# Kernel optimization log

Hardware: AMD Instinct MI355X
Metric: run time of the kernel (lower is better)

The kernel has to match this reference:

```python
import jax, jax.numpy as jnp
import numpy as np

KERNEL = 3
STRIDE = 1

def _unfold(x, k, s):
    # torch.nn.Unfold: output [B, C*k*k, P] with (c, kh, kw) flattened channel-major
    B, C, H, W = x.shape
    oh = (H - k) // s + 1
    ow = (W - k) // s + 1
    cols = []
    for di in range(k):
        for dj in range(k):
            cols.append(x[:, :, di:di + oh * s:s, dj:dj + ow * s:s])
    p = jnp.stack(cols, axis=2)            # [B, C, k*k, oh, ow]
    return p.reshape(B, C * k * k, oh * ow), oh, ow

def setup_inputs() -> dict:
    key = jax.random.key(0)
    k1, k2 = jax.random.split(key)
    B, C, H, W = 32, 96, 32, 32
    out_c, k, s = 96, KERNEL, STRIDE
    oh = (H - k) // s + 1
    ow = (W - k) // s + 1
    P = oh * ow
    x = jax.random.normal(k1, (B, C, H, W), dtype=jnp.float32)
    weight = jax.random.normal(k2, (P, out_c, C * k * k), dtype=jnp.float32) * 0.01
    bias = jnp.zeros((P, out_c), dtype=jnp.float32)
    return {"x": x, "weight": weight, "bias": bias}

def reference(x, weight, bias):
    B = x.shape[0]
    out_c = weight.shape[1]
    patches, oh, ow = _unfold(x, KERNEL, STRIDE)          # [B, K, P]
    # per-patch distinct weights: out[b,p,o] = sum_k patches[b,k,p] * weight[p,o,k]
    out = jnp.einsum('bkp,pok->bpo', patches, weight) + bias[None, :, :]
    out = out.transpose(0, 2, 1).reshape(B, out_c, oh, ow)
    return out
```

## Files before the change

kernel.cpp:

```cpp
#include <hip/hip_runtime.h>


namespace {
constexpr int BATCH = 32;
constexpr int CIN   = 96;
constexpr int HIN   = 32;
constexpr int WIN   = 32;
constexpr int OC    = 96;
constexpr int OH    = 30;
constexpr int OW    = 30;
constexpr int NP    = OH * OW;
constexpr int KTOT  = CIN * 9;
constexpr int KC    = 72;
constexpr int NCH   = KTOT / KC;
constexpr int NTHR  = 192;
constexpr int APAD  = 36;
constexpr int WPAD  = 100;
}

__global__ __launch_bounds__(NTHR, 3)
void lc_forward(const float* __restrict__ x,
                const float* __restrict__ weight,
                const float* __restrict__ bias,
                float* __restrict__ out)
{
    __shared__ float Alds[KC][APAD];
    __shared__ float Wlds[KC][WPAD];

    const int p    = blockIdx.x;
    const int pi   = p / OW;
    const int pj   = p - pi * OW;
    const int t    = threadIdx.x;
    const int lane = t & 63;
    const int wv   = t >> 6;

    const int b0 = (lane >> 3) << 2;
    const int o0 = wv * 32 + ((lane & 7) << 2);

    float acc[4][4] = {};

    const float* wp    = weight + (size_t)p * (OC * KTOT);
    const float* xbase = x + pi * WIN + pj;

    for (int ch = 0; ch < NCH; ++ch) {
        #pragma unroll
        for (int it = 0; it < (BATCH * KC) / NTHR; ++it) {
            const int e  = t + it * NTHR;
            const int b  = e / KC;
            const int rm = e - b * KC;
            const int cc = rm / 9;
            const int r  = rm - cc * 9;
            const int di = r / 3;
            const int dj = r - di * 3;
            Alds[rm][b] = xbase[(size_t)b * (CIN * HIN * WIN)
                                + (ch * 8 + cc) * (HIN * WIN)
                                + di * WIN + dj];
        }
        const float* wc = wp + ch * KC;
        #pragma unroll
        for (int it = 0; it < (OC * KC / 4) / NTHR; ++it) {
            const int f  = t + it * NTHR;
            const int o  = f / (KC / 4);
            const int kq = f - o * (KC / 4);
            const float4 v = *reinterpret_cast<const float4*>(wc + (size_t)o * KTOT + (kq << 2));
            const int kk = kq << 2;
            Wlds[kk + 0][o] = v.x;
            Wlds[kk + 1][o] = v.y;
            Wlds[kk + 2][o] = v.z;
            Wlds[kk + 3][o] = v.w;
        }
        __syncthreads();

        #pragma unroll 4
        for (int kk = 0; kk < KC; ++kk) {
            const float4 a = *reinterpret_cast<const float4*>(&Alds[kk][b0]);
            const float4 w = *reinterpret_cast<const float4*>(&Wlds[kk][o0]);
            acc[0][0] = fmaf(a.x, w.x, acc[0][0]);
            acc[0][1] = fmaf(a.x, w.y, acc[0][1]);
            acc[0][2] = fmaf(a.x, w.z, acc[0][2]);
            acc[0][3] = fmaf(a.x, w.w, acc[0][3]);
            acc[1][0] = fmaf(a.y, w.x, acc[1][0]);
            acc[1][1] = fmaf(a.y, w.y, acc[1][1]);
            acc[1][2] = fmaf(a.y, w.z, acc[1][2]);
            acc[1][3] = fmaf(a.y, w.w, acc[1][3]);
            acc[2][0] = fmaf(a.z, w.x, acc[2][0]);
            acc[2][1] = fmaf(a.z, w.y, acc[2][1]);
            acc[2][2] = fmaf(a.z, w.z, acc[2][2]);
            acc[2][3] = fmaf(a.z, w.w, acc[2][3]);
            acc[3][0] = fmaf(a.w, w.x, acc[3][0]);
            acc[3][1] = fmaf(a.w, w.y, acc[3][1]);
            acc[3][2] = fmaf(a.w, w.z, acc[3][2]);
            acc[3][3] = fmaf(a.w, w.w, acc[3][3]);
        }
        __syncthreads();
    }

    const float* bp = bias + (size_t)p * OC;
    #pragma unroll
    for (int i = 0; i < 4; ++i) {
        #pragma unroll
        for (int j = 0; j < 4; ++j) {
            out[((size_t)(b0 + i) * OC + (o0 + j)) * NP + p] = acc[i][j] + bp[o0 + j];
        }
    }
}

extern "C" void kernel_launch(void* const* d_in, const int* in_sizes, int n_in,
                              void* d_out, int out_size, void* d_ws, size_t ws_size,
                              hipStream_t stream) {
    const float* x  = (const float*)d_in[0];
    const float* w  = (const float*)d_in[1];
    const float* bi = (const float*)d_in[2];
    float* o        = (float*)d_out;
    lc_forward<<<dim3(NP), dim3(NTHR), 0, stream>>>(x, w, bi, o);
}
```

Baseline: 489.2 us.

## Split output channels across blocks, load weights directly to registers, prefetch patches

Each patch position is now split into two blocks of 48 output channels. Weights are read straight from global memory into registers as float4, so the weight LDS buffer and its transpose are gone. The next patch chunk is prefetched into registers while the current one is computed, and a block-id swizzle spreads work across XCDs. The goal is to cut LDS traffic and LDS use so more blocks fit per CU (launch bounds raised to 5). The cost is that weight loads are strided per thread rather than coalesced, and each block reloads the input patches.

```diff
diff --git a/kernel.cpp b/kernel.cpp
--- a/kernel.cpp
+++ b/kernel.cpp
@@ -2,107 +2,114 @@
 
 
 namespace {
-constexpr int BATCH = 32;
 constexpr int CIN   = 96;
-constexpr int HIN   = 32;
-constexpr int WIN   = 32;
+constexpr int HW_   = 1024;
+constexpr int CSTR  = CIN * HW_;
 constexpr int OC    = 96;
-constexpr int OH    = 30;
 constexpr int OW    = 30;
-constexpr int NP    = OH * OW;
-constexpr int KTOT  = CIN * 9;
-constexpr int KC    = 72;
+constexpr int NP    = 900;
+constexpr int KTOT  = 864;
+constexpr int KC    = 108;
 constexpr int NCH   = KTOT / KC;
 constexpr int NTHR  = 192;
 constexpr int APAD  = 36;
-constexpr int WPAD  = 100;
+constexpr int OBLK  = 48;
+constexpr int NBLK  = NP * 2;
+constexpr int CHUNK = NBLK / 8;
 }
 
-__global__ __launch_bounds__(NTHR, 3)
+__global__ __launch_bounds__(NTHR, 5)
 void lc_forward(const float* __restrict__ x,
                 const float* __restrict__ weight,
                 const float* __restrict__ bias,
                 float* __restrict__ out)
 {
     __shared__ float Alds[KC][APAD];
-    __shared__ float Wlds[KC][WPAD];
 
-    const int p    = blockIdx.x;
-    const int pi   = p / OW;
-    const int pj   = p - pi * OW;
+    const int bid = blockIdx.x;
+    const int swz = (bid & 7) * CHUNK + (bid >> 3);
+    const int oh  = swz / NP;
+    const int p   = swz - oh * NP;
+    const int pi  = p / OW;
+    const int pj  = p - pi * OW;
+
     const int t    = threadIdx.x;
     const int lane = t & 63;
     const int wv   = t >> 6;
 
-    const int b0 = (lane >> 3) << 2;
-    const int o0 = wv * 32 + ((lane & 7) << 2);
+    const int b0  = (lane & 15) * 2;
+    const int og  = wv * 4 + (lane >> 4);
+    const int o0g = oh * OBLK + og * 4;
 
-    float acc[4][4] = {};
+    const int bs  = t & 31;
+    const int rm0 = t >> 5;
 
-    const float* wp    = weight + (size_t)p * (OC * KTOT);
-    const float* xbase = x + pi * WIN + pj;
+    const float* xb    = x + (size_t)bs * CSTR + pi * 32 + pj;
+    const float* wbase = weight + ((size_t)p * OC + o0g) * KTOT;
+
+    float acc0[4] = {0.f, 0.f, 0.f, 0.f};
+    float acc1[4] = {0.f, 0.f, 0.f, 0.f};
+    float xr[18];
+
+#define LOADX(CH)                                         \
+    {                                                     \
+        _Pragma("unroll")                                 \
+        for (int j = 0; j < 18; ++j) {                    \
+            const int ka = (CH) * KC + rm0 + 6 * j;       \
+            const int c  = ka / 9;                        \
+            const int r  = ka - c * 9;                    \
+            const int di = r / 3;                         \
+            const int dj = r - di * 3;                    \
+            xr[j] = xb[c * HW_ + di * 32 + dj];           \
+        }                                                 \
+    }
+
+    LOADX(0);
 
     for (int ch = 0; ch < NCH; ++ch) {
+        __syncthreads();
         #pragma unroll
-        for (int it = 0; it < (BATCH * KC) / NTHR; ++it) {
-            const int e  = t + it * NTHR;
-            const int b  = e / KC;
-            const int rm = e - b * KC;
-            const int cc = rm / 9;
-            const int r  = rm - cc * 9;
-            const int di = r / 3;
-            const int dj = r - di * 3;
-            Alds[rm][b] = xbase[(size_t)b * (CIN * HIN * WIN)
-                                + (ch * 8 + cc) * (HIN * WIN)
-                                + di * WIN + dj];
+        for (int j = 0; j < 18; ++j)
+            Alds[rm0 + 6 * j][bs] = xr[j];
+        __syncthreads();
+        if (ch < NCH - 1) LOADX(ch + 1);
+
+        const float* wch = wbase + ch * KC;
+        #pragma unroll
+        for (int kq = 0; kq < KC / 4; ++kq) {
+            const float4 w0 = *reinterpret_cast<const float4*>(wch + 0 * KTOT + kq * 4);
+            const float4 w1 = *reinterpret_cast<const float4*>(wch + 1 * KTOT + kq * 4);
+            const float4 w2 = *reinterpret_cast<const float4*>(wch + 2 * KTOT + kq * 4);
+            const float4 w3 = *reinterpret_cast<const float4*>(wch + 3 * KTOT + kq * 4);
+            const float2 a0 = *reinterpret_cast<const float2*>(&Alds[kq * 4 + 0][b0]);
+            const float2 a1 = *reinterpret_cast<const float2*>(&Alds[kq * 4 + 1][b0]);
+            const float2 a2 = *reinterpret_cast<const float2*>(&Alds[kq * 4 + 2][b0]);
+            const float2 a3 = *reinterpret_cast<const float2*>(&Alds[kq * 4 + 3][b0]);
+#define COLJ(J, WJ)                                                         \
+            acc0[J] = fmaf(a0.x, WJ.x, acc0[J]);                            \
+            acc1[J] = fmaf(a0.y, WJ.x, acc1[J]);                            \
+            acc0[J] = fmaf(a1.x, WJ.y, acc0[J]);                            \
+            acc1[J] = fmaf(a1.y, WJ.y, acc1[J]);                            \
+            acc0[J] = fmaf(a2.x, WJ.z, acc0[J]);                            \
+            acc1[J] = fmaf(a2.y, WJ.z, acc1[J]);                            \
+            acc0[J] = fmaf(a3.x, WJ.w, acc0[J]);                            \
+            acc1[J] = fmaf(a3.y, WJ.w, acc1[J]);
+            COLJ(0, w0)
+            COLJ(1, w1)
+            COLJ(2, w2)
+            COLJ(3, w3)
+#undef COLJ
         }
-        const float* wc = wp + ch * KC;
-        #pragma unroll
-        for (int it = 0; it < (OC * KC / 4) / NTHR; ++it) {
-            const int f  = t + it * NTHR;
-            const int o  = f / (KC / 4);
-            const int kq = f - o * (KC / 4);
-            const float4 v = *reinterpret_cast<const float4*>(wc + (size_t)o * KTOT + (kq << 2));
-            const int kk = kq << 2;
-            Wlds[kk + 0][o] = v.x;
-            Wlds[kk + 1][o] = v.y;
-            Wlds[kk + 2][o] = v.z;
-            Wlds[kk + 3][o] = v.w;
-        }
-        __syncthreads();
-
-        #pragma unroll 4
-        for (int kk = 0; kk < KC; ++kk) {
-            const float4 a = *reinterpret_cast<const float4*>(&Alds[kk][b0]);
-            const float4 w = *reinterpret_cast<const float4*>(&Wlds[kk][o0]);
-            acc[0][0] = fmaf(a.x, w.x, acc[0][0]);
-            acc[0][1] = fmaf(a.x, w.y, acc[0][1]);
-            acc[0][2] = fmaf(a.x, w.z, acc[0][2]);
-            acc[0][3] = fmaf(a.x, w.w, acc[0][3]);
-            acc[1][0] = fmaf(a.y, w.x, acc[1][0]);
-            acc[1][1] = fmaf(a.y, w.y, acc[1][1]);
-            acc[1][2] = fmaf(a.y, w.z, acc[1][2]);
-            acc[1][3] = fmaf(a.y, w.w, acc[1][3]);
-            acc[2][0] = fmaf(a.z, w.x, acc[2][0]);
-            acc[2][1] = fmaf(a.z, w.y, acc[2][1]);
-            acc[2][2] = fmaf(a.z, w.z, acc[2][2]);
-            acc[2][3] = fmaf(a.z, w.w, acc[2][3]);
-            acc[3][0] = fmaf(a.w, w.x, acc[3][0]);
-            acc[3][1] = fmaf(a.w, w.y, acc[3][1]);
-            acc[3][2] = fmaf(a.w, w.z, acc[3][2]);
-            acc[3][3] = fmaf(a.w, w.w, acc[3][3]);
-        }
-        __syncthreads();
     }
 
-    const float* bp = bias + (size_t)p * OC;
+    const float* bp = bias + (size_t)p * OC + o0g;
     #pragma unroll
-    for (int i = 0; i < 4; ++i) {
-        #pragma unroll
-        for (int j = 0; j < 4; ++j) {
-            out[((size_t)(b0 + i) * OC + (o0 + j)) * NP + p] = acc[i][j] + bp[o0 + j];
-        }
+    for (int j = 0; j < 4; ++j) {
+        const float bb = bp[j];
+        out[((size_t)(b0 + 0) * OC + o0g + j) * NP + p] = acc0[j] + bb;
+        out[((size_t)(b0 + 1) * OC + o0g + j) * NP + p] = acc1[j] + bb;
     }
+#undef LOADX
 }
 
 extern "C" void kernel_launch(void* const* d_in, const int* in_sizes, int n_in,
@@ -112,5 +119,5 @@
     const float* w  = (const float*)d_in[1];
     const float* bi = (const float*)d_in[2];
     float* o        = (float*)d_out;
-    lc_forward<<<dim3(NP), dim3(NTHR), 0, stream>>>(x, w, bi, o);
+    lc_forward<<<dim3(NBLK), dim3(NTHR), 0, stream>>>(x, w, bi, o);
 }
```

Result: slower. 796.0 us (+62.7%).

## Switch per-patch GEMM to bf16 MFMA with staged output and transpose kernel

Applied to the files above, without the earlier changes.

Replaces the fp32 FMA outer-product GEMM with bf16 16x16x32 MFMA instructions. Patch values are converted to bf16 and packed into LDS in fragment layout, while weights are read straight from global memory into registers and converted there. Each patch is now split into two blocks by output-channel half. Results go to a workspace in [p][b][o] layout, and a separate tiled transpose kernel writes the final layout, replacing the strided scattered stores. Converting to bf16 lowers precision, and the second launch and workspace round-trip add memory traffic.

```diff
diff --git a/kernel.cpp b/kernel.cpp
--- a/kernel.cpp
+++ b/kernel.cpp
@@ -2,106 +2,127 @@
 
 
 namespace {
-constexpr int BATCH = 32;
-constexpr int CIN   = 96;
-constexpr int HIN   = 32;
-constexpr int WIN   = 32;
-constexpr int OC    = 96;
-constexpr int OH    = 30;
-constexpr int OW    = 30;
-constexpr int NP    = OH * OW;
-constexpr int KTOT  = CIN * 9;
-constexpr int KC    = 72;
-constexpr int NCH   = KTOT / KC;
-constexpr int NTHR  = 192;
-constexpr int APAD  = 36;
-constexpr int WPAD  = 100;
+constexpr int CIN  = 96;
+constexpr int HW_  = 1024;
+constexpr int CSTR = CIN * HW_;
+constexpr int OC   = 96;
+constexpr int OW   = 30;
+constexpr int NP   = 900;
+constexpr int KTOT = 864;
+constexpr int KC   = 288;
+constexpr int NCH  = KTOT / KC;
+constexpr int NTHR = 192;
+constexpr int NBLK = NP * 2;
 }
 
-__global__ __launch_bounds__(NTHR, 3)
-void lc_forward(const float* __restrict__ x,
-                const float* __restrict__ weight,
-                const float* __restrict__ bias,
-                float* __restrict__ out)
+typedef __attribute__((ext_vector_type(8))) short   bf16x8;
+typedef __attribute__((ext_vector_type(4))) float   f32x4;
+
+__device__ __forceinline__ unsigned short f2bf(float f) {
+    unsigned u = __builtin_bit_cast(unsigned, f);
+    u += 0x7fffu + ((u >> 16) & 1u);
+    return (unsigned short)(u >> 16);
+}
+
+__global__ __launch_bounds__(NTHR, 6)
+void lc_mfma(const float* __restrict__ x, const float* __restrict__ weight,
+             const float* __restrict__ bias, float* __restrict__ ws)
 {
-    __shared__ float Alds[KC][APAD];
-    __shared__ float Wlds[KC][WPAD];
+    __shared__ unsigned Albuf[9 * 2 * 64 * 4];
 
-    const int p    = blockIdx.x;
-    const int pi   = p / OW;
-    const int pj   = p - pi * OW;
+    const int bid = blockIdx.x;
+    const int p   = bid >> 1;
+    const int oh  = bid & 1;
+    const int pi  = p / OW;
+    const int pj  = p - pi * OW;
+
     const int t    = threadIdx.x;
     const int lane = t & 63;
     const int wv   = t >> 6;
 
-    const int b0 = (lane >> 3) << 2;
-    const int o0 = wv * 32 + ((lane & 7) << 2);
+    const int nlane = lane & 15;
+    const int kq    = lane >> 4;
+    const int o_ln  = oh * 48 + wv * 16 + nlane;
+    const float* wrow = weight + ((size_t)p * OC + o_ln) * KTOT + (kq << 3);
+    const float  bb   = bias[(size_t)p * OC + o_ln];
 
-    float acc[4][4] = {};
+    const int bs   = t & 31;
+    const int kset = t >> 5;
+    const int mt_s = bs >> 4;
+    const int bl   = bs & 15;
+    const float* xb = x + (size_t)bs * CSTR + pi * 32 + pj;
 
-    const float* wp    = weight + (size_t)p * (OC * KTOT);
-    const float* xbase = x + pi * WIN + pj;
+    f32x4 acc0 = {0.f, 0.f, 0.f, 0.f};
+    f32x4 acc1 = {0.f, 0.f, 0.f, 0.f};
 
     for (int ch = 0; ch < NCH; ++ch) {
-        #pragma unroll
-        for (int it = 0; it < (BATCH * KC) / NTHR; ++it) {
-            const int e  = t + it * NTHR;
-            const int b  = e / KC;
-            const int rm = e - b * KC;
-            const int cc = rm / 9;
-            const int r  = rm - cc * 9;
-            const int di = r / 3;
-            const int dj = r - di * 3;
-            Alds[rm][b] = xbase[(size_t)b * (CIN * HIN * WIN)
-                                + (ch * 8 + cc) * (HIN * WIN)
-                                + di * WIN + dj];
-        }
-        const float* wc = wp + ch * KC;
-        #pragma unroll
-        for (int it = 0; it < (OC * KC / 4) / NTHR; ++it) {
-            const int f  = t + it * NTHR;
-            const int o  = f / (KC / 4);
-            const int kq = f - o * (KC / 4);
-            const float4 v = *reinterpret_cast<const float4*>(wc + (size_t)o * KTOT + (kq << 2));
-            const int kk = kq << 2;
-            Wlds[kk + 0][o] = v.x;
-            Wlds[kk + 1][o] = v.y;
-            Wlds[kk + 2][o] = v.z;
-            Wlds[kk + 3][o] = v.w;
+        if (ch) __syncthreads();
+        const float* xc = xb + ch * 32 * HW_;
+        #pragma unroll 6
+        for (int j = 0; j < 24; ++j) {
+            const int kk = 2 * kset + 12 * j;
+            const int k1 = kk + 1;
+            const int c0 = kk / 9, r0 = kk - 9 * c0, di0 = r0 / 3, dj0 = r0 - 3 * di0;
+            const int c1 = k1 / 9, r1 = k1 - 9 * c1, di1 = r1 / 3, dj1 = r1 - 3 * di1;
+            const float f0 = xc[c0 * HW_ + di0 * 32 + dj0];
+            const float f1 = xc[c1 * HW_ + di1 * 32 + dj1];
+            const int s  = kk >> 5;
+            const int ke = kk & 31;
+            const int lw = bl + ((ke >> 3) << 4);
+            const int e  = ke & 7;
+            const int off = (((s * 2 + mt_s) * 64 + lw) << 3) + e;
+            Albuf[off >> 1] = (unsigned)f2bf(f0) | ((unsigned)f2bf(f1) << 16);
         }
         __syncthreads();
 
-        #pragma unroll 4
-        for (int kk = 0; kk < KC; ++kk) {
-            const float4 a = *reinterpret_cast<const float4*>(&Alds[kk][b0]);
-            const float4 w = *reinterpret_cast<const float4*>(&Wlds[kk][o0]);
-            acc[0][0] = fmaf(a.x, w.x, acc[0][0]);
-            acc[0][1] = fmaf(a.x, w.y, acc[0][1]);
-            acc[0][2] = fmaf(a.x, w.z, acc[0][2]);
-            acc[0][3] = fmaf(a.x, w.w, acc[0][3]);
-            acc[1][0] = fmaf(a.y, w.x, acc[1][0]);
-            acc[1][1] = fmaf(a.y, w.y, acc[1][1]);
-            acc[1][2] = fmaf(a.y, w.z, acc[1][2]);
-            acc[1][3] = fmaf(a.y, w.w, acc[1][3]);
-            acc[2][0] = fmaf(a.z, w.x, acc[2][0]);
-            acc[2][1] = fmaf(a.z, w.y, acc[2][1]);
-            acc[2][2] = fmaf(a.z, w.z, acc[2][2]);
-            acc[2][3] = fmaf(a.z, w.w, acc[2][3]);
-            acc[3][0] = fmaf(a.w, w.x, acc[3][0]);
-            acc[3][1] = fmaf(a.w, w.y, acc[3][1]);
-            acc[3][2] = fmaf(a.w, w.z, acc[3][2]);
-            acc[3][3] = fmaf(a.w, w.w, acc[3][3]);
+        const bf16x8* Afr = (const bf16x8*)Albuf;
+        #pragma unroll 3
+        for (int s = 0; s < 9; ++s) {
+            const int ks = ch * 9 + s;
+            const float4 wlo = *(const float4*)(wrow + ks * 32);
+            const float4 whi = *(const float4*)(wrow + ks * 32 + 4);
+            bf16x8 bfr;
+            bfr[0] = (short)f2bf(wlo.x); bfr[1] = (short)f2bf(wlo.y);
+            bfr[2] = (short)f2bf(wlo.z); bfr[3] = (short)f2bf(wlo.w);
+            bfr[4] = (short)f2bf(whi.x); bfr[5] = (short)f2bf(whi.y);
+            bfr[6] = (short)f2bf(whi.z); bfr[7] = (short)f2bf(whi.w);
+            const bf16x8 a0 = Afr[(s * 2 + 0) * 64 + lane];
+            const bf16x8 a1 = Afr[(s * 2 + 1) * 64 + lane];
+            acc0 = __builtin_amdgcn_mfma_f32_16x16x32_bf16(a0, bfr, acc0, 0, 0, 0);
+            acc1 = __builtin_amdgcn_mfma_f32_16x16x32_bf16(a1, bfr, acc1, 0, 0, 0);
         }
-        __syncthreads();
     }
 
-    const float* bp = bias + (size_t)p * OC;
+    float* wsp = ws + (size_t)p * (32 * OC);
     #pragma unroll
-    for (int i = 0; i < 4; ++i) {
-        #pragma unroll
-        for (int j = 0; j < 4; ++j) {
-            out[((size_t)(b0 + i) * OC + (o0 + j)) * NP + p] = acc[i][j] + bp[o0 + j];
-        }
+    for (int r = 0; r < 4; ++r) {
+        const int brow = (kq << 2) + r;
+        wsp[(size_t)brow * OC + o_ln]        = acc0[r] + bb;
+        wsp[(size_t)(16 + brow) * OC + o_ln] = acc1[r] + bb;
+    }
+}
+
+__global__ __launch_bounds__(256)
+void lc_transpose(const float* __restrict__ ws, float* __restrict__ out)
+{
+    __shared__ float tile[64][65];
+    const int bo0 = blockIdx.x * 64;
+    const int p0  = blockIdx.y * 64;
+    const int tx  = threadIdx.x & 63;
+    const int ty  = threadIdx.x >> 6;
+
+    #pragma unroll
+    for (int i = 0; i < 16; ++i) {
+        const int pp = i * 4 + ty;
+        if (p0 + pp < NP)
+            tile[pp][tx] = ws[(size_t)(p0 + pp) * 3072 + bo0 + tx];
+    }
+    __syncthreads();
+    #pragma unroll
+    for (int i = 0; i < 16; ++i) {
+        const int bb = i * 4 + ty;
+        if (p0 + tx < NP)
+            out[(size_t)(bo0 + bb) * NP + p0 + tx] = tile[tx][bb];
     }
 }
 
@@ -111,6 +132,9 @@
     const float* x  = (const float*)d_in[0];
     const float* w  = (const float*)d_in[1];
     const float* bi = (const float*)d_in[2];
-    float* o        = (float*)d_out;
-    lc_forward<<<dim3(NP), dim3(NTHR), 0, stream>>>(x, w, bi, o);
+    float* out      = (float*)d_out;
+    float* ws       = (float*)d_ws;
+
+    lc_mfma<<<dim3(NBLK), dim3(NTHR), 0, stream>>>(x, w, bi, ws);
+    lc_transpose<<<dim3(3072 / 64, (NP + 63) / 64), dim3(256), 0, stream>>>(ws, out);
 }
```

Measured after the change: 578.6 us. +18.3%, slower.
